# Optimization experiments

Hardware: AMD Instinct MI355X
Metric: run time of the kernel (lower is better)

The kernel has to match this reference:

```python
import jax, jax.numpy as jnp
import numpy as np

B, IN, OUT, M = 4096, 512, 512, 16


def setup_inputs() -> dict:
    key = jax.random.key(0)
    k1, k2, k3 = jax.random.split(key, 3)
    # inputs kept strictly positive and inside the physical range [0, 60]
    x = jax.random.uniform(k1, (B, IN), jnp.float32, 0.1, 10.0)
    # photonic basis coefficients: positive, with small polynomial terms
    b_coef = jax.random.uniform(k2, (M, 8), jnp.float32, 0.1, 0.9)
    b_coef = b_coef.at[:, 4:].multiply(0.01)
    coeffs = 0.01 * jax.random.normal(k3, (OUT, IN, M), jnp.float32)
    return {"x": x, "coeffs": coeffs, "b_coef": b_coef}


def _photonic_basis(x, b):
    # x: (B, IN) -> broadcast against M basis functions -> (B, IN, M)
    xe = x[:, :, None]                                   # (B, IN, 1)
    b1, b2, b3, b4, b5, b6, b7, b8 = [b[:, i][None, None, :] for i in range(8)]
    inner = jnp.expm1(b3 * xe)
    powered = jnp.power(inner, b4)
    y = (b1 * jnp.log(1.0 + b2 * jnp.log1p(powered))
         + b5 * xe + b6 * xe**2 + b7 * xe**3 + b8 * xe**4)
    return y


def reference(x, coeffs, b_coef):
    # basis: (B, IN, M); double reduce over (IN, M) == GEMM of size B x (IN*M) x OUT
    basis = _photonic_basis(x, b_coef)
    y = jnp.einsum('bim,oim->bo', basis, coeffs)         # (B, OUT)
    return y
```

## Files before the change

### kernel.cpp

```cpp
#include <hip/hip_runtime.h>
#include <hip/hip_bf16.h>
#include <stdint.h>

#define B_DIM   4096
#define IN_DIM  512
#define OUT_DIM 512
#define M_DIM   16
#define K_DIM   (IN_DIM * M_DIM)
#define MN      (B_DIM * OUT_DIM)

typedef unsigned short ushort_t;
typedef __attribute__((ext_vector_type(8))) __bf16 bf16x8;
typedef __attribute__((ext_vector_type(2))) __bf16 bf16x2;
typedef __attribute__((ext_vector_type(4))) float  f32x4;

__device__ __forceinline__ ushort_t f2bf(float f) {
  union { float f; uint32_t u; } v; v.f = f;
  uint32_t u = v.u + 0x7fffu + ((v.u >> 16) & 1u);
  return (ushort_t)(u >> 16);
}

__device__ __forceinline__ uint32_t pkbf(float lo, float hi) {
  union { bf16x2 h; uint32_t u; } v;
  v.h[0] = (__bf16)lo; v.h[1] = (__bf16)hi;
  return v.u;
}

__device__ __forceinline__ float rfl(float f) {
  union { float f; int i; } v; v.f = f;
  v.i = __builtin_amdgcn_readfirstlane(v.i);
  return v.f;
}

#define CONV_N4 (OUT_DIM * K_DIM / 4)
__global__ __launch_bounds__(256) void convert_coeffs_kernel(
    const float* __restrict__ src, ushort_t* __restrict__ dst) {
  int i = blockIdx.x * 256 + threadIdx.x;
  float4 v = ((const float4*)src)[i];
  ushort4 o;
  o.x = f2bf(v.x); o.y = f2bf(v.y); o.z = f2bf(v.z); o.w = f2bf(v.w);
  ((ushort4*)dst)[i] = o;
}

#define BM 128
#define BN 512
#define BK 32
#define SPLITK 8
#define KC (K_DIM / SPLITK)
#define NITER (KC / BK)
#define XCOLS (KC / M_DIM)
#define XPAD  129

#define GLD16(g, l) \
  __builtin_amdgcn_global_load_lds((const __attribute__((address_space(1))) void*)(g), \
                                   (__attribute__((address_space(3))) void*)(l), 16, 0, 0)

#define WAIT_BAR(N) \
  asm volatile("s_waitcnt vmcnt(" #N ") lgkmcnt(0)\n\ts_barrier" ::: "memory")

template <int ATOMIC>
__global__ __launch_bounds__(512, 2) void gemm_kernel(
    const float* __restrict__ x,
    const ushort_t* __restrict__ Bt,
    const float* __restrict__ bc,
    float* __restrict__ P) {
  __shared__ __align__(16) ushort_t As[2][BM * BK];
  __shared__ __align__(16) ushort_t Bs[3][BN * BK];
  __shared__ __align__(16) float    Xs[XCOLS * XPAD];
  const int tid  = threadIdx.x;
  const int wave = tid >> 6;
  const int lane = tid & 63;
  const int wgid = blockIdx.x;
  const int ks = wgid & 7, bm = wgid >> 3;

  {
    const int r = tid >> 2, q = tid & 3;
    const float4* xrow = (const float4*)(x + (size_t)(bm * BM + r) * IN_DIM + ks * XCOLS);
    #pragma unroll
    for (int j = 0; j < 4; ++j) {
      float4 v = xrow[q * 4 + j];
      Xs[(q * 16 + j * 4 + 0) * XPAD + r] = v.x;
      Xs[(q * 16 + j * 4 + 1) * XPAD + r] = v.y;
      Xs[(q * 16 + j * 4 + 2) * XPAD + r] = v.z;
      Xs[(q * 16 + j * 4 + 3) * XPAD + r] = v.w;
    }
  }

  const int srow = wave * 16 + (lane >> 2);
  const int scol = (((lane & 3) ^ ((lane >> 3) & 3)) * 8);
  const ushort_t* Bg0 = Bt + (size_t)srow * K_DIM + ks * KC + scol;
  const ushort_t* Bg1 = Bg0 + (size_t)128 * K_DIM;
  const ushort_t* Bg2 = Bg0 + (size_t)256 * K_DIM;
  const ushort_t* Bg3 = Bg0 + (size_t)384 * K_DIM;
  const int bofs0 = (wave * 16) * BK;
  const int bofs1 = (128 + wave * 16) * BK;
  const int bofs2 = (256 + wave * 16) * BK;
  const int bofs3 = (384 + wave * 16) * BK;

#define STAGEB(lb) do { \
    GLD16(Bg0, &Bs[lb][bofs0]); GLD16(Bg1, &Bs[lb][bofs1]); \
    GLD16(Bg2, &Bs[lb][bofs2]); GLD16(Bg3, &Bs[lb][bofs3]); \
    Bg0 += BK; Bg1 += BK; Bg2 += BK; Bg3 += BK; } while (0)

  const int half = wave & 1;
  const int arow = (wave >> 1) * 32 + (lane >> 1);
  const int il   = lane & 1;
  const int aslot = ((il * 2 + half) ^ ((lane >> 2) & 3));
  const int awe   = arow * BK + aslot * 8;
  const int xbase = il * XPAD + arow;

  const float LOG2E = 1.44269504088896340736f;
  const float LN2   = 0.69314718055994530942f;
  float c1[8], c2[8], c3[8], c4[8], c5[8], c6[8], c7[8], c8[8];
  {
    const float* bch = bc + half * 64;
    #pragma unroll
    for (int m = 0; m < 8; ++m) {
      c1[m] = rfl(rfl(bch[m*8+0]) * LN2); c2[m] = rfl(rfl(bch[m*8+1]) * LN2);
      c3[m] = rfl(bch[m*8+2]); c4[m] = rfl(bch[m*8+3]);
      c5[m] = rfl(bch[m*8+4]); c6[m] = rfl(bch[m*8+5]);
      c7[m] = rfl(bch[m*8+6]); c8[m] = rfl(bch[m*8+7]);
    }
  }

#define BASIS(ab, t) do { \
    float xv = Xs[xbase + 2 * XPAD * (t)]; \
    float xl2 = xv * LOG2E; \
    float x2 = xv * xv, x3 = x2 * xv, x4 = x2 * x2; \
    float ym[8]; \
    _Pragma("unroll") \
    for (int mi = 0; mi < 8; ++mi) { \
      float e     = __builtin_amdgcn_exp2f(c3[mi] * xl2); \
      float inner = e - 1.0f; \
      float p     = __builtin_amdgcn_exp2f(c4[mi] * __builtin_amdgcn_logf(inner)); \
      float L1    = __builtin_amdgcn_logf(1.0f + p); \
      float vv    = __builtin_amdgcn_logf(1.0f + c2[mi] * L1); \
      ym[mi] = c1[mi] * vv + c5[mi] * xv + c6[mi] * x2 + c7[mi] * x3 + c8[mi] * x4; \
    } \
    *(uint4*)(&As[ab][awe]) = make_uint4(pkbf(ym[0], ym[1]), pkbf(ym[2], ym[3]), \
                                         pkbf(ym[4], ym[5]), pkbf(ym[6], ym[7])); \
  } while (0)

  const int wr = wave >> 2, wc = wave & 3;
  const int fm = lane & 15;
  const int fkswz = (((lane >> 4) ^ ((lane >> 1) & 3)) << 3);

  f32x4 acc[4][8] = {};

#define COMPUTE(ab, lb) do { \
    bf16x8 af[4], bfv[8]; \
    _Pragma("unroll") \
    for (int t2 = 0; t2 < 4; ++t2) \
      af[t2] = *(const bf16x8*)&As[ab][(wr * 64 + t2 * 16 + fm) * BK + fkswz]; \
    _Pragma("unroll") \
    for (int u = 0; u < 8; ++u) \
      bfv[u] = *(const bf16x8*)&Bs[lb][(wc * 128 + u * 16 + fm) * BK + fkswz]; \
    __builtin_amdgcn_s_setprio(1); \
    _Pragma("unroll") \
    for (int mt = 0; mt < 4; ++mt) \
      _Pragma("unroll") \
      for (int nt = 0; nt < 8; ++nt) \
        acc[mt][nt] = __builtin_amdgcn_mfma_f32_16x16x32_bf16(af[mt], bfv[nt], acc[mt][nt], 0, 0, 0); \
    __builtin_amdgcn_s_setprio(0); \
  } while (0)

#define STEP(lbN, ap, ac, lb, t1) do { \
    STAGEB(lbN); BASIS(ap, t1); COMPUTE(ac, lb); WAIT_BAR(4); } while (0)

  STAGEB(0); STAGEB(1);
  __syncthreads();
  BASIS(0, 0);
  WAIT_BAR(0);

  for (int tb = 0; tb < NITER - 2; tb += 6) {
    STEP(2, 1, 0, 0, tb + 1);
    STEP(0, 0, 1, 1, tb + 2);
    STEP(1, 1, 0, 2, tb + 3);
    STEP(2, 0, 1, 0, tb + 4);
    STEP(0, 1, 0, 1, tb + 5);
    STEP(1, 0, 1, 2, tb + 6);
  }
  BASIS(1, NITER - 1);
  COMPUTE(0, 0);
  WAIT_BAR(0);
  COMPUTE(1, 1);

  const int colb = wc * 128 + fm;
  const int rowb = bm * BM + wr * 64 + (lane >> 4) * 4;
  float* out = P + (ATOMIC ? (size_t)0 : (size_t)ks * MN);
  #pragma unroll
  for (int mt = 0; mt < 4; ++mt) {
    #pragma unroll
    for (int nt = 0; nt < 8; ++nt) {
      #pragma unroll
      for (int j = 0; j < 4; ++j) {
        int row = rowb + mt * 16 + j;
        int col = colb + nt * 16;
        float vv = acc[mt][nt][j];
        if (ATOMIC) atomicAdd(out + (size_t)row * OUT_DIM + col, vv);
        else        out[(size_t)row * OUT_DIM + col] = vv;
      }
    }
  }
#undef STAGEB
#undef BASIS
#undef COMPUTE
#undef STEP
}

__global__ __launch_bounds__(256) void reduce_kernel(
    const float* __restrict__ P, float* __restrict__ out) {
  int i = blockIdx.x * 256 + threadIdx.x;
  const float4* p = (const float4*)P;
  float4 r = p[i];
  #pragma unroll
  for (int s = 1; s < SPLITK; ++s) {
    float4 v = p[i + (size_t)s * (MN / 4)];
    r.x += v.x; r.y += v.y; r.z += v.z; r.w += v.w;
  }
  ((float4*)out)[i] = r;
}

extern "C" void kernel_launch(void* const* d_in, const int* in_sizes, int n_in,
                              void* d_out, int out_size, void* d_ws, size_t ws_size,
                              hipStream_t stream) {
  const float* x      = (const float*)d_in[0];
  const float* coeffs = (const float*)d_in[1];
  const float* b_coef = (const float*)d_in[2];
  float* out = (float*)d_out;
  char*  ws  = (char*)d_ws;

  const size_t COEF_BYTES = (size_t)OUT_DIM * K_DIM * 2;
  ushort_t* coefb = (ushort_t*)ws;
  float* partials = (float*)(ws + COEF_BYTES);
  const size_t FULL = COEF_BYTES + (size_t)SPLITK * MN * 4;
  const bool use_atomic = (ws_size < FULL);

  convert_coeffs_kernel<<<CONV_N4 / 256, 256, 0, stream>>>(coeffs, coefb);

  const int nblk = (B_DIM / BM) * SPLITK;
  if (use_atomic) {
    hipMemsetAsync(d_out, 0, (size_t)MN * 4, stream);
    gemm_kernel<1><<<nblk, 512, 0, stream>>>(x, coefb, b_coef, out);
  } else {
    gemm_kernel<0><<<nblk, 512, 0, stream>>>(x, coefb, b_coef, partials);
    reduce_kernel<<<MN / 4 / 256, 256, 0, stream>>>(partials, out);
  }
}
```

Baseline: 135.0 us.

## Fuse split-K reduction into GEMM via last-arriving workgroup counter

Removes the separate reduce kernel. Each GEMM workgroup bumps a per-row-block atomic counter after writing its partial tile, and the last of the SPLITK workgroups sums all partials for that 128-row block and writes the output. This saves a kernel launch and lets the reduction overlap with GEMM work still running in other blocks, at the cost of a memset for the counters, extra fences, and a serial tail handled by whichever workgroup finishes last.

```diff
diff --git a/kernel.cpp b/kernel.cpp
--- a/kernel.cpp
+++ b/kernel.cpp
@@ -63,10 +63,13 @@
     const float* __restrict__ x,
     const ushort_t* __restrict__ Bt,
     const float* __restrict__ bc,
-    float* __restrict__ P) {
+    float* __restrict__ P,
+    float* __restrict__ outF,
+    int* __restrict__ ctr) {
   __shared__ __align__(16) ushort_t As[2][BM * BK];
   __shared__ __align__(16) ushort_t Bs[3][BN * BK];
   __shared__ __align__(16) float    Xs[XCOLS * XPAD];
+  __shared__ int lastArr;
   const int tid  = threadIdx.x;
   const int wave = tid >> 6;
   const int lane = tid & 63;
@@ -187,7 +190,7 @@
 
   const int colb = wc * 128 + fm;
   const int rowb = bm * BM + wr * 64 + (lane >> 4) * 4;
-  float* out = P + (ATOMIC ? (size_t)0 : (size_t)ks * MN);
+  float* dst = ATOMIC ? outF : (P + (size_t)ks * MN);
   #pragma unroll
   for (int mt = 0; mt < 4; ++mt) {
     #pragma unroll
@@ -197,8 +200,32 @@
         int row = rowb + mt * 16 + j;
         int col = colb + nt * 16;
         float vv = acc[mt][nt][j];
-        if (ATOMIC) atomicAdd(out + (size_t)row * OUT_DIM + col, vv);
-        else        out[(size_t)row * OUT_DIM + col] = vv;
+        if (ATOMIC) atomicAdd(dst + (size_t)row * OUT_DIM + col, vv);
+        else        dst[(size_t)row * OUT_DIM + col] = vv;
+      }
+    }
+  }
+
+  if (!ATOMIC) {
+    __threadfence();
+    __syncthreads();
+    if (tid == 0) lastArr = (atomicAdd(&ctr[bm], 1) == SPLITK - 1);
+    __syncthreads();
+    if (lastArr) {
+      __threadfence();
+      const size_t base4 = (size_t)bm * (BM * OUT_DIM / 4);
+      const float4* p4 = (const float4*)P;
+      float4* o4 = (float4*)outF;
+      #pragma unroll 4
+      for (int it = 0; it < (BM * OUT_DIM / 4) / 512; ++it) {
+        size_t idx = base4 + (size_t)it * 512 + tid;
+        float4 r = p4[idx];
+        #pragma unroll
+        for (int s = 1; s < SPLITK; ++s) {
+          float4 v = p4[idx + (size_t)s * (MN / 4)];
+          r.x += v.x; r.y += v.y; r.z += v.z; r.w += v.w;
+        }
+        o4[idx] = r;
       }
     }
   }
@@ -206,19 +233,6 @@
 #undef BASIS
 #undef COMPUTE
 #undef STEP
-}
-
-__global__ __launch_bounds__(256) void reduce_kernel(
-    const float* __restrict__ P, float* __restrict__ out) {
-  int i = blockIdx.x * 256 + threadIdx.x;
-  const float4* p = (const float4*)P;
-  float4 r = p[i];
-  #pragma unroll
-  for (int s = 1; s < SPLITK; ++s) {
-    float4 v = p[i + (size_t)s * (MN / 4)];
-    r.x += v.x; r.y += v.y; r.z += v.z; r.w += v.w;
-  }
-  ((float4*)out)[i] = r;
 }
 
 extern "C" void kernel_launch(void* const* d_in, const int* in_sizes, int n_in,
@@ -231,9 +245,11 @@
   char*  ws  = (char*)d_ws;
 
   const size_t COEF_BYTES = (size_t)OUT_DIM * K_DIM * 2;
+  const size_t PART_BYTES = (size_t)SPLITK * MN * 4;
   ushort_t* coefb = (ushort_t*)ws;
   float* partials = (float*)(ws + COEF_BYTES);
-  const size_t FULL = COEF_BYTES + (size_t)SPLITK * MN * 4;
+  int*   ctr      = (int*)(ws + COEF_BYTES + PART_BYTES);
+  const size_t FULL = COEF_BYTES + PART_BYTES + (B_DIM / BM) * sizeof(int);
   const bool use_atomic = (ws_size < FULL);
 
   convert_coeffs_kernel<<<CONV_N4 / 256, 256, 0, stream>>>(coeffs, coefb);
@@ -241,9 +257,9 @@
   const int nblk = (B_DIM / BM) * SPLITK;
   if (use_atomic) {
     hipMemsetAsync(d_out, 0, (size_t)MN * 4, stream);
-    gemm_kernel<1><<<nblk, 512, 0, stream>>>(x, coefb, b_coef, out);
+    gemm_kernel<1><<<nblk, 512, 0, stream>>>(x, coefb, b_coef, out, out, nullptr);
   } else {
-    gemm_kernel<0><<<nblk, 512, 0, stream>>>(x, coefb, b_coef, partials);
-    reduce_kernel<<<MN / 4 / 256, 256, 0, stream>>>(partials, out);
-  }
-}
+    hipMemsetAsync(ctr, 0, (B_DIM / BM) * sizeof(int), stream);
+    gemm_kernel<0><<<nblk, 512, 0, stream>>>(x, coefb, b_coef, partials, out, ctr);
+  }
+}
```

Measured after the change: 251.0 us. +85.9%, slower.
